# Kernel optimization log

Measured on AMD Instinct MI355X. Metric: run time of the kernel, lower is better.

The kernel has to match this reference:

```python
import jax, jax.numpy as jnp
import numpy as np

HEADS = 4

def gat_layer(x, W, a_src, a_dst, bias, edge_index, n):
    # PyG-style GATConv with self-loops, heads averaged (concat=False) so out dim == hidden_dim
    H, C = a_src.shape
    h = (x @ W).reshape(n, H, C)                      # [N,H,C]
    loops = jnp.arange(n)
    src = jnp.concatenate([edge_index[0], loops])
    dst = jnp.concatenate([edge_index[1], loops])
    e = jax.nn.leaky_relu((h * a_src).sum(-1)[src] + (h * a_dst).sum(-1)[dst], 0.2)  # [E,H]
    m = jax.ops.segment_max(e, dst, num_segments=n)   # segment softmax over incoming edges
    ex = jnp.exp(e - m[dst])
    s = jax.ops.segment_sum(ex, dst, num_segments=n)
    alpha = ex / (s[dst] + 1e-16)
    out = jax.ops.segment_sum(alpha[:, :, None] * h[src], dst, num_segments=n)  # [N,H,C]
    return out.mean(axis=1) + bias

def setup_inputs() -> dict:
    key = jax.random.key(0)
    ks = jax.random.split(key, 24)
    Nd, Ni, Ne = 20000, 4096, 4096
    D_in, D = 512, 256
    n_int, n_emo = 64, 32
    inp = {}
    inp['dialogue_embeddings'] = jax.random.normal(ks[0], (Nd, D_in), jnp.float32)
    inp['intention_indices'] = jax.random.randint(ks[1], (Ni,), 0, n_int)
    inp['emotion_indices'] = jax.random.randint(ks[2], (Ne,), 0, n_emo)
    inp['dialogue_edge_index'] = jax.random.randint(ks[3], (2, Nd * 32), 0, Nd)
    inp['intention_edge_index'] = jax.random.randint(ks[4], (2, Ni * 16), 0, Ni)
    inp['emotion_edge_index'] = jax.random.randint(ks[5], (2, Ne * 16), 0, Ne)
    s = lambda k, shape: jax.random.normal(k, shape, jnp.float32) * 0.02
    inp['intention_emb'] = s(ks[6], (n_int, D))
    inp['emotion_emb'] = s(ks[7], (n_emo, D))
    inp['Wd'] = s(ks[8], (D_in, HEADS * D)); inp['a_src_d'] = s(ks[9], (HEADS, D)); inp['a_dst_d'] = s(ks[10], (HEADS, D)); inp['bd'] = jnp.zeros((D,), jnp.float32)
    inp['Wi'] = s(ks[11], (D, HEADS * D)); inp['a_src_i'] = s(ks[12], (HEADS, D)); inp['a_dst_i'] = s(ks[13], (HEADS, D)); inp['bi'] = jnp.zeros((D,), jnp.float32)
    inp['We'] = s(ks[14], (D, HEADS * D)); inp['a_src_e'] = s(ks[15], (HEADS, D)); inp['a_dst_e'] = s(ks[16], (HEADS, D)); inp['be'] = jnp.zeros((D,), jnp.float32)
    inp['W_dfc'] = s(ks[17], (D, D)); inp['b_dfc'] = jnp.zeros((D,), jnp.float32)
    inp['W_ifc'] = s(ks[18], (D, D)); inp['b_ifc'] = jnp.zeros((D,), jnp.float32)
    inp['W_efc'] = s(ks[19], (D, D)); inp['b_efc'] = jnp.zeros((D,), jnp.float32)
    inp['W_fc'] = s(ks[20], (3 * D, n_emo)); inp['b_fc'] = jnp.zeros((n_emo,), jnp.float32)
    return inp

def reference(dialogue_embeddings, intention_indices, emotion_indices,
              dialogue_edge_index, intention_edge_index, emotion_edge_index,
              intention_emb, emotion_emb,
              Wd, a_src_d, a_dst_d, bd, Wi, a_src_i, a_dst_i, bi,
              We, a_src_e, a_dst_e, be,
              W_dfc, b_dfc, W_ifc, b_ifc, W_efc, b_efc, W_fc, b_fc):
    Nd = dialogue_embeddings.shape[0]
    Ni = intention_indices.shape[0]
    Ne = emotion_indices.shape[0]
    ie = intention_emb[intention_indices]   # [Ni, D]
    ee = emotion_emb[emotion_indices]       # [Ne, D]
    d = gat_layer(dialogue_embeddings, Wd, a_src_d, a_dst_d, bd, dialogue_edge_index, Nd)
    d = jax.nn.relu(d @ W_dfc + b_dfc)
    i = gat_layer(ie, Wi, a_src_i, a_dst_i, bi, intention_edge_index, Ni)
    i = jax.nn.relu(i @ W_ifc + b_ifc)
    e = gat_layer(ee, We, a_src_e, a_dst_e, be, emotion_edge_index, Ne)
    e = jax.nn.relu(e @ W_efc + b_efc)
    iw = jax.nn.softmax(d @ i.T, axis=-1)   # [Nd, Ni]
    att_i = iw @ i                           # [Nd, D]
    ew = jax.nn.softmax(d @ e.T, axis=-1)   # [Nd, Ne]
    att_e = ew @ e                           # [Nd, D]
    inputs = jnp.concatenate([d, att_i, att_e], axis=-1)  # [Nd, 3D]
    return inputs @ W_fc + b_fc
```

## Files before the change

kernel.cpp:

```cpp
#include <hip/hip_runtime.h>
#include <hip/hip_bf16.h>
#include <math.h>

#define DEV static __device__ __forceinline__

typedef __attribute__((ext_vector_type(8))) short short8;
typedef __attribute__((ext_vector_type(4))) short short4v;
typedef __attribute__((ext_vector_type(4))) float f32x4;
typedef __attribute__((ext_vector_type(2))) long long2v;

DEV float bf2f(__hip_bfloat16 x) { return __bfloat162float(x); }
DEV __hip_bfloat16 f2bf(float x) { return __float2bfloat16(x); }
DEV short bfbits(float x) { __hip_bfloat16 h = __float2bfloat16(x); short s; __builtin_memcpy(&s, &h, 2); return s; }
DEV float b2f_bits(short s) { __hip_bfloat16 h; __builtin_memcpy(&h, &s, 2); return __bfloat162float(h); }
DEV float lrelu(float x) { return x > 0.f ? x : 0.2f * x; }

DEV float load_in(const void* p, long long i, bool f32) {
  return f32 ? ((const float*)p)[i] : bf2f(((const __hip_bfloat16*)p)[i]);
}

DEV long pack8_fp8(const float* f) {
  int lo = 0, hi = 0;
  lo = __builtin_amdgcn_cvt_pk_fp8_f32(f[0], f[1], lo, false);
  lo = __builtin_amdgcn_cvt_pk_fp8_f32(f[2], f[3], lo, true);
  hi = __builtin_amdgcn_cvt_pk_fp8_f32(f[4], f[5], hi, false);
  hi = __builtin_amdgcn_cvt_pk_fp8_f32(f[6], f[7], hi, true);
  return ((long)(unsigned)hi << 32) | (unsigned)lo;
}

DEV f32x4 mfma_fp8(long a, long b, f32x4 c) {
  return __builtin_amdgcn_mfma_f32_16x16x32_fp8_fp8(a, b, c, 0, 0, 0);
}

__global__ void HGAN_45148696215914_kernel() {}

__global__ void fill_k(__hip_bfloat16* __restrict__ p, float v, int n)
{
  int i = blockIdx.x * blockDim.x + threadIdx.x;
  if (i < n) p[i] = __float2bfloat16(v);
}

struct DetectArgs { const unsigned int* p[23]; int nw[23]; int id[23]; };

__global__ void detect_k(DetectArgs a, int* __restrict__ flags)
{
  __shared__ int cnt_sh;
  if (threadIdx.x == 0) cnt_sh = 0;
  __syncthreads();
  const unsigned int* w = a.p[blockIdx.x];
  int nwords = a.nw[blockIdx.x];
  int bad = 0;
  for (int i = threadIdx.x; i < nwords; i += blockDim.x) {
    unsigned int x = w[i];
    float v0 = __uint_as_float((x & 0xffffu) << 16);
    float v1 = __uint_as_float(x & 0xffff0000u);
    if (!(fabsf(v0) <= 1e4f)) bad++;
    if (!(fabsf(v1) <= 1e4f)) bad++;
  }
  atomicAdd(&cnt_sh, bad);
  __syncthreads();
  if (threadIdx.x == 0) flags[a.id[blockIdx.x]] = (cnt_sh > nwords / 4) ? 1 : 0;
}

struct CvArgs {
  const void* in[7]; const int* flag[7]; __hip_bfloat16* out[7];
  int K[7], N[7], NL[7], toff[7]; int nseg;
};

__global__ __launch_bounds__(256) void convtrN_k(CvArgs a)
{
  __shared__ __hip_bfloat16 t[32][33];
  int b = blockIdx.x;
  int s = 0;
  while (s + 1 < a.nseg && b >= a.toff[s + 1]) ++s;
  int ti = b - a.toff[s];
  int kb = a.K[s] >> 5;
  int bk = ti % kb, bn = ti / kb;
  const void* in = a.in[s];
  const int* flag = a.flag[s];
  __hip_bfloat16* out = a.out[s];
  int K = a.K[s], N = a.N[s];
  const bool f = flag && *flag;
  int lx = threadIdx.x & 31, ly = threadIdx.x >> 5;
  int gn = bn * 32 + lx;
#pragma unroll
  for (int rr = 0; rr < 32; rr += 8)
    t[rr + ly][lx] = (gn < N)
        ? f2bf(load_in(in, (long long)(bk * 32 + rr + ly) * N + gn, f))
        : f2bf(0.f);
  __syncthreads();
#pragma unroll
  for (int rr = 0; rr < 32; rr += 8)
    out[(size_t)(bn * 32 + rr + ly) * K + bk * 32 + lx] = t[lx][rr + ly];
}

DEV void mgemm_body(
    const void* A, const int* aflag, int lda, const int* idxA,
    const __hip_bfloat16* BT, void* C, int ldc,
    const void* bias, const int* biasflag, int relu,
    int permC, int M, int K, int Nlim, const int* cflag,
    int m0, int n0, __hip_bfloat16* Ash, __hip_bfloat16* Bsh)
{
  const bool af = aflag && *aflag;
  const bool bsf = biasflag && *biasflag;
  const bool cf = cflag && *cflag;
  const int tid = threadIdx.x;
  const int wv = tid >> 6, lane = tid & 63, qd = lane >> 4, lm = lane & 15;
  const int wr = wv >> 1, wc = wv & 1;

  f32x4 acc[4][4];
#pragma unroll
  for (int i = 0; i < 4; ++i)
    for (int j = 0; j < 4; ++j)
      for (int v = 0; v < 4; ++v) acc[i][j][v] = 0.f;

  for (int k0 = 0; k0 < K; k0 += 64) {
    __syncthreads();
    for (int u = tid; u < 1024; u += 256) {
      int r = u >> 3, cu = u & 7;
      int gm = m0 + r;
      short8 vv;
      if (gm < M) {
        long long row = idxA ? idxA[gm] : gm;
        long long basei = row * (long long)lda + k0 + cu * 8;
        if (af) {
          const float4* fp = (const float4*)((const float*)A + basei);
          float4 f0 = fp[0], f1 = fp[1];
          vv[0] = bfbits(f0.x); vv[1] = bfbits(f0.y);
          vv[2] = bfbits(f0.z); vv[3] = bfbits(f0.w);
          vv[4] = bfbits(f1.x); vv[5] = bfbits(f1.y);
          vv[6] = bfbits(f1.z); vv[7] = bfbits(f1.w);
        } else {
          vv = *(const short8*)((const __hip_bfloat16*)A + basei);
        }
      } else {
#pragma unroll
        for (int j = 0; j < 8; ++j) vv[j] = 0;
      }
      *(short8*)(&Ash[r * 72 + cu * 8]) = vv;
    }
    for (int u = tid; u < 1024; u += 256) {
      int r = u >> 3, cu = u & 7;
      *(short8*)(&Bsh[r * 72 + cu * 8]) =
          *(const short8*)(BT + (size_t)(n0 + r) * K + k0 + cu * 8);
    }
    __syncthreads();
#pragma unroll
    for (int ks = 0; ks < 2; ++ks) {
      short8 a[4], b[4];
#pragma unroll
      for (int i = 0; i < 4; ++i)
        a[i] = *(const short8*)(&Ash[(wr * 64 + i * 16 + lm) * 72 + ks * 32 + qd * 8]);
#pragma unroll
      for (int j = 0; j < 4; ++j)
        b[j] = *(const short8*)(&Bsh[(wc * 64 + j * 16 + lm) * 72 + ks * 32 + qd * 8]);
#pragma unroll
      for (int i = 0; i < 4; ++i)
#pragma unroll
        for (int j = 0; j < 4; ++j)
          acc[i][j] = __builtin_amdgcn_mfma_f32_16x16x32_bf16(a[i], b[j], acc[i][j], 0, 0, 0);
    }
  }
#pragma unroll
  for (int j = 0; j < 4; ++j) {
    int gn = n0 + wc * 64 + j * 16 + lm;
    if (gn >= Nlim) continue;
    float bv = bias ? load_in(bias, gn, bsf) : 0.f;
    int gcol = permC ? ((gn & 255) * 4 + (gn >> 8)) : gn;
#pragma unroll
    for (int i = 0; i < 4; ++i) {
#pragma unroll
      for (int v = 0; v < 4; ++v) {
        int gm = m0 + wr * 64 + i * 16 + qd * 4 + v;
        if (gm >= M) continue;
        float x = acc[i][j][v] + bv;
        if (relu) x = fmaxf(x, 0.f);
        long long idx = (long long)gm * ldc + gcol;
        if (cf) ((float*)C)[idx] = x;
        else    ((__hip_bfloat16*)C)[idx] = f2bf(x);
      }
    }
  }
}

__global__ __launch_bounds__(256) void mgemm_k(
    const void* __restrict__ A, const int* __restrict__ aflag, int lda,
    const int* __restrict__ idxA,
    const __hip_bfloat16* __restrict__ BT,
    void* __restrict__ C, int ldc,
    const void* __restrict__ bias, const int* __restrict__ biasflag, int relu,
    int permC, int M, int N, int K, int Nlim,
    const int* __restrict__ cflag)
{
  __shared__ __align__(16) __hip_bfloat16 Ash[128 * 72];
  __shared__ __align__(16) __hip_bfloat16 Bsh[128 * 72];
  (void)N;
  mgemm_body(A, aflag, lda, idxA, BT, C, ldc, bias, biasflag, relu,
             permC, M, K, Nlim, cflag,
             blockIdx.y * 128, blockIdx.x * 128, Ash, Bsh);
}

struct SegArgs {
  const void* A[3]; const int* aflag[3]; int lda[3]; const int* idxA[3];
  const __hip_bfloat16* BT[3]; void* C[3]; int ldc[3];
  const void* bias[3]; const int* bflag[3];
  int M[3]; int K[3]; int yoff[3];
  int relu, permC, Nlim;
};

__global__ __launch_bounds__(256) void mgemm_seg_k(SegArgs a)
{
  __shared__ __align__(16) __hip_bfloat16 Ash[128 * 72];
  __shared__ __align__(16) __hip_bfloat16 Bsh[128 * 72];
  int y = blockIdx.y;
  int s = (y >= a.yoff[2]) ? 2 : ((y >= a.yoff[1]) ? 1 : 0);
  mgemm_body(a.A[s], a.aflag[s], a.lda[s], a.idxA[s], a.BT[s], a.C[s], a.ldc[s],
             a.bias[s], a.bflag[s], a.relu, a.permC, a.M[s], a.K[s], a.Nlim,
             nullptr, (y - a.yoff[s]) * 128, blockIdx.x * 128, Ash, Bsh);
}

__global__ __launch_bounds__(256) void score3_k(
    const __hip_bfloat16* __restrict__ hI,
    const void* as1, const void* ad1, const int* sf1, const int* df1,
    const void* as2, const void* ad2, const int* sf2, const int* df2,
    const void* as3, const void* ad3, const int* sf3, const int* df3,
    int s1, int s2,
    float* __restrict__ ss, float* __restrict__ ds,
    int* __restrict__ cnt, int N)
{
  __shared__ float red[4][8];
  int n = blockIdx.x, c = threadIdx.x;
  if (c == 0) cnt[n] = 0;
  const void* a_src; const void* a_dst; const int* sfp; const int* dfp;
  if (n < s1)      { a_src = as1; a_dst = ad1; sfp = sf1; dfp = df1; }
  else if (n < s2) { a_src = as2; a_dst = ad2; sfp = sf2; dfp = df2; }
  else             { a_src = as3; a_dst = ad3; sfp = sf3; dfp = df3; }
  const bool sf = sfp && *sfp;
  const bool df = dfp && *dfp;
  short4v hv = *(const short4v*)(hI + (size_t)n * 1024 + c * 4);
  float h0 = b2f_bits(hv[0]), h1 = b2f_bits(hv[1]);
  float h2 = b2f_bits(hv[2]), h3 = b2f_bits(hv[3]);
  float r0 = h0 * load_in(a_src, 0 * 256 + c, sf);
  float r1 = h1 * load_in(a_src, 1 * 256 + c, sf);
  float r2 = h2 * load_in(a_src, 2 * 256 + c, sf);
  float r3 = h3 * load_in(a_src, 3 * 256 + c, sf);
  float t0 = h0 * load_in(a_dst, 0 * 256 + c, df);
  float t1 = h1 * load_in(a_dst, 1 * 256 + c, df);
  float t2 = h2 * load_in(a_dst, 2 * 256 + c, df);
  float t3 = h3 * load_in(a_dst, 3 * 256 + c, df);
#pragma unroll
  for (int o = 32; o > 0; o >>= 1) {
    r0 += __shfl_down(r0, o); r1 += __shfl_down(r1, o);
    r2 += __shfl_down(r2, o); r3 += __shfl_down(r3, o);
    t0 += __shfl_down(t0, o); t1 += __shfl_down(t1, o);
    t2 += __shfl_down(t2, o); t3 += __shfl_down(t3, o);
  }
  int wv = c >> 6, lane = c & 63;
  if (lane == 0) {
    red[wv][0] = r0; red[wv][1] = r1; red[wv][2] = r2; red[wv][3] = r3;
    red[wv][4] = t0; red[wv][5] = t1; red[wv][6] = t2; red[wv][7] = t3;
  }
  __syncthreads();
  if (c < 8) {
    float s = red[0][c] + red[1][c] + red[2][c] + red[3][c];
    if (c < 4) ss[n * 4 + c] = s;
    else       ds[n * 4 + (c - 4)] = s;
  }
}

__global__ void count3_k(const int* __restrict__ d1, int E1,
                         const int* __restrict__ d2, int E2, int o2,
                         const int* __restrict__ d3, int E3, int o3,
                         int* __restrict__ cnt)
{
  int k = blockIdx.x * blockDim.x + threadIdx.x;
  if (k < E1) atomicAdd(&cnt[d1[k]], 1);
  else if (k < E1 + E2) atomicAdd(&cnt[d2[k - E1] + o2], 1);
  else if (k < E1 + E2 + E3) atomicAdd(&cnt[d3[k - E1 - E2] + o3], 1);
}

__global__ __launch_bounds__(1024) void scan1_k(
    const int* __restrict__ cnt, int* __restrict__ offp, int* __restrict__ bsum, int n)
{
  __shared__ int sh[1024];
  int idx = blockIdx.x * 1024 + (int)threadIdx.x;
  int v = (idx < n) ? cnt[idx] : 0;
  sh[threadIdx.x] = v;
  __syncthreads();
  for (int d = 1; d < 1024; d <<= 1) {
    int t = (threadIdx.x >= (unsigned)d) ? sh[threadIdx.x - d] : 0;
    __syncthreads();
    sh[threadIdx.x] += t;
    __syncthreads();
  }
  if (idx < n) offp[idx] = sh[threadIdx.x] - v;
  if (threadIdx.x == 1023) bsum[blockIdx.x] = sh[1023];
}

__global__ void scan3_k(int* __restrict__ offp, const int* __restrict__ bsum,
                        int* __restrict__ cur, int n, int nb)
{
  int i = blockIdx.x * blockDim.x + threadIdx.x;
  if (i < n) {
    int chunk = i >> 10;
    int pre = 0;
    for (int b = 0; b < chunk; ++b) pre += bsum[b];
    int v = offp[i] + pre;
    offp[i] = v;
    cur[i] = v;
    if (i == n - 1) {
      int tot = 0;
      for (int b = 0; b < nb; ++b) tot += bsum[b];
      offp[n] = tot;
    }
  }
}

__global__ void scatter3_k(const int* __restrict__ s1, const int* __restrict__ d1, int E1,
                           const int* __restrict__ s2, const int* __restrict__ d2, int E2, int o2,
                           const int* __restrict__ s3, const int* __restrict__ d3, int E3, int o3,
                           int* __restrict__ cur, int* __restrict__ srcs)
{
  int k = blockIdx.x * blockDim.x + threadIdx.x;
  if (k < E1) {
    int p = atomicAdd(&cur[d1[k]], 1);
    srcs[p] = s1[k];
  } else if (k < E1 + E2) {
    int kk = k - E1;
    int p = atomicAdd(&cur[d2[kk] + o2], 1);
    srcs[p] = s2[kk] + o2;
  } else if (k < E1 + E2 + E3) {
    int kk = k - E1 - E2;
    int p = atomicAdd(&cur[d3[kk] + o3], 1);
    srcs[p] = s3[kk] + o3;
  }
}

__global__ __launch_bounds__(256) void agg3_k(
    const __hip_bfloat16* __restrict__ hI,
    const float* __restrict__ ss, const float* __restrict__ ds,
    const int* __restrict__ offp, const int* __restrict__ srcs,
    const void* b1, const int* bf1,
    const void* b2, const int* bf2,
    const void* b3, const int* bf3,
    int s1, int s2,
    __hip_bfloat16* __restrict__ outp, int N)
{
  __shared__ int src_sh[64];
  __shared__ __align__(16) float w_sh[64][4];
  __shared__ float scale_sh[4];
  __shared__ float l_sh[4];
  __shared__ __align__(16) float pair_sh[128][8];
  int n = blockIdx.x;
  int c = threadIdx.x;
  int hd_w = c >> 6;
  int e_w  = c & 63;
  int half = c >> 7;
  int tc   = c & 127;
  int s0 = offp[n], deg = offp[n + 1] - s0;
  int total = deg + 1;
  float dsn = ds[n * 4 + hd_w];
  float m_run = -1e30f, l_run = 0.f;
  float A0[4] = {0.f, 0.f, 0.f, 0.f};
  float A1[4] = {0.f, 0.f, 0.f, 0.f};
  for (int base = 0; base < total; base += 64) {
    int cnt = min(64, total - base);
    __syncthreads();
    if (c < cnt) src_sh[c] = (base + c == 0) ? n : srcs[s0 + base + c - 1];
    __syncthreads();
    float val = -1e30f;
    if (e_w < cnt) val = lrelu(ss[src_sh[e_w] * 4 + hd_w] + dsn);
    float vmax = val;
#pragma unroll
    for (int o = 32; o > 0; o >>= 1) vmax = fmaxf(vmax, __shfl_xor(vmax, o));
    float newm = fmaxf(m_run, vmax);
    float p = (e_w < cnt) ? __expf(val - newm) : 0.f;
    float psum = p;
#pragma unroll
    for (int o = 32; o > 0; o >>= 1) psum += __shfl_xor(psum, o);
    float sc = __expf(m_run - newm);
    l_run = l_run * sc + psum;
    m_run = newm;
    w_sh[e_w][hd_w] = p;
    if (e_w == 0) scale_sh[hd_w] = sc;
    __syncthreads();
    float sc0 = scale_sh[0], sc1 = scale_sh[1], sc2 = scale_sh[2], sc3 = scale_sh[3];
    A0[0] *= sc0; A0[1] *= sc1; A0[2] *= sc2; A0[3] *= sc3;
    A1[0] *= sc0; A1[1] *= sc1; A1[2] *= sc2; A1[3] *= sc3;
    for (int e = half; e < cnt; e += 2) {
      short8 hv = *(const short8*)(hI + (size_t)src_sh[e] * 1024 + tc * 8);
      float4 w = *(const float4*)(&w_sh[e][0]);
      A0[0] += w.x * b2f_bits(hv[0]); A0[1] += w.y * b2f_bits(hv[1]);
      A0[2] += w.z * b2f_bits(hv[2]); A0[3] += w.w * b2f_bits(hv[3]);
      A1[0] += w.x * b2f_bits(hv[4]); A1[1] += w.y * b2f_bits(hv[5]);
      A1[2] += w.z * b2f_bits(hv[6]); A1[3] += w.w * b2f_bits(hv[7]);
    }
  }
  __syncthreads();
  if (e_w == 0) l_sh[hd_w] = l_run;
  if (half == 1) {
    *(float4*)(&pair_sh[tc][0]) = make_float4(A0[0], A0[1], A0[2], A0[3]);
    *(float4*)(&pair_sh[tc][4]) = make_float4(A1[0], A1[1], A1[2], A1[3]);
  }
  __syncthreads();
  if (half == 0) {
    float4 p0 = *(const float4*)(&pair_sh[tc][0]);
    float4 p1 = *(const float4*)(&pair_sh[tc][4]);
    A0[0] += p0.x; A0[1] += p0.y; A0[2] += p0.z; A0[3] += p0.w;
    A1[0] += p1.x; A1[1] += p1.y; A1[2] += p1.z; A1[3] += p1.w;
    const void* bias; const int* bfp;
    if (n < s1)      { bias = b1; bfp = bf1; }
    else if (n < s2) { bias = b2; bfp = bf2; }
    else             { bias = b3; bfp = bf3; }
    const bool bf = bfp && *bfp;
    float il0 = 1.f / (l_sh[0] + 1e-16f), il1 = 1.f / (l_sh[1] + 1e-16f);
    float il2 = 1.f / (l_sh[2] + 1e-16f), il3 = 1.f / (l_sh[3] + 1e-16f);
    float r0 = 0.25f * (A0[0] * il0 + A0[1] * il1 + A0[2] * il2 + A0[3] * il3);
    float r1 = 0.25f * (A1[0] * il0 + A1[1] * il1 + A1[2] * il2 + A1[3] * il3);
    outp[(size_t)n * 256 + 2 * tc]     = f2bf(r0 + load_in(bias, 2 * tc, bf));
    outp[(size_t)n * 256 + 2 * tc + 1] = f2bf(r1 + load_in(bias, 2 * tc + 1, bf));
  }
}

__global__ __launch_bounds__(256) void conv8_k(
    const __hip_bfloat16* __restrict__ in0, char* __restrict__ K8_0, char* __restrict__ KT8_0,
    const __hip_bfloat16* __restrict__ in1, char* __restrict__ K8_1, char* __restrict__ KT8_1,
    int Nk)
{
  __shared__ __align__(16) __hip_bfloat16 t[32][264];
  const __hip_bfloat16* in = blockIdx.y ? in1 : in0;
  char* K8  = blockIdx.y ? K8_1  : K8_0;
  char* KT8 = blockIdx.y ? KT8_1 : KT8_0;
  int kv0 = blockIdx.x * 32;
  size_t tbase = (size_t)(kv0 >> 5) * 8192;
  int tid = threadIdx.x;
  (void)Nk;
  for (int u = tid; u < 1024; u += 256) {
    int r = u >> 5, c = u & 31;
    *(short8*)(&t[r][c * 8]) = *(const short8*)(in + (size_t)(kv0 + r) * 256 + c * 8);
  }
  __syncthreads();
  for (int u = tid; u < 1024; u += 256) {
    int r = u >> 5, g = u & 31, pos = g * 8;
    int qd_ = pos >> 6, s = (pos >> 3) & 7;
    int d = s * 32 + qd_ * 8;
    float f[8];
#pragma unroll
    for (int j = 0; j < 8; ++j) f[j] = 16.f * bf2f(t[r][d + j]);
    int c16 = pos >> 4, h = (pos >> 3) & 1;
    int unit = ((c16 & 3) * 2 + (r >> 4)) * 64 + (c16 >> 2) * 16 + (r & 15);
    *(long*)(K8 + tbase + (size_t)unit * 16 + h * 8) = pack8_fp8(f);
  }
  {
    int d = tid;
#pragma unroll
    for (int g = 0; g < 4; ++g) {
      float f[8];
#pragma unroll
      for (int j = 0; j < 8; ++j) f[j] = 16.f * bf2f(t[g * 8 + j][d]);
      int unit = (d >> 4) * 64 + g * 16 + (d & 15);
      *(long*)(KT8 + tbase + (size_t)unit * 8) = pack8_fp8(f);
    }
  }
}

__global__ __launch_bounds__(512, 4) void flashf8_k(
    const __hip_bfloat16* __restrict__ Q, int ldq,
    const char* __restrict__ K8_0, const char* __restrict__ KT8_0,
    const char* __restrict__ K8_1, const char* __restrict__ KT8_1,
    __hip_bfloat16* __restrict__ Out, int ldo,
    int M, int Nk)
{
  __shared__ __align__(16) char Ksh8[2][8192];
  __shared__ __align__(16) char KTsh8[2][8192];
  __shared__ __align__(16) char Psh8[8][16 * 40];
  const int att = blockIdx.y;
  const char* K8  = att ? K8_1  : K8_0;
  const char* KT8 = att ? KT8_1 : KT8_0;
  __hip_bfloat16* Outp = Out + att * 256;

  const int tid = threadIdx.x;
  const int wv = tid >> 6, lane = tid & 63;
  const int qd = lane >> 4, lm = lane & 15;
  const int r0 = blockIdx.x * 128 + wv * 16;
  char* Pw = Psh8[wv];

  long qf8[8];
  {
    const bool ok = (r0 + lm) < M;
    const __hip_bfloat16* qrow = Q + (size_t)(r0 + lm) * ldq;
#pragma unroll
    for (int s = 0; s < 8; ++s) {
      float f[8];
      if (ok) {
        short8 qv = *(const short8*)(qrow + s * 32 + qd * 8);
#pragma unroll
        for (int j = 0; j < 8; ++j) f[j] = 16.f * b2f_bits(qv[j]);
      } else {
#pragma unroll
        for (int j = 0; j < 8; ++j) f[j] = 0.f;
      }
      qf8[s] = pack8_fp8(f);
    }
  }

  f32x4 Oacc[16];
#pragma unroll
  for (int i = 0; i < 16; ++i)
    for (int v = 0; v < 4; ++v) Oacc[i][v] = 0.f;
  float mrow = -1e30f, lrow = 0.f;

  {
    short8 k0 = *(const short8*)(K8 + (size_t)tid * 16);
    short8 t0 = *(const short8*)(KT8 + (size_t)tid * 16);
    *(short8*)(&Ksh8[0][tid * 16]) = k0;
    *(short8*)(&KTsh8[0][tid * 16]) = t0;
  }
  __syncthreads();

  int iter = 0;
  for (int n0 = 0; n0 < Nk; n0 += 32, ++iter) {
    const int cur = iter & 1, nxt = cur ^ 1;
    const bool havenext = (n0 + 32) < Nk;
    short8 pk0, pt0;
    if (havenext) {
      size_t tb = (size_t)(iter + 1) * 8192;
      pk0 = *(const short8*)(K8 + tb + (size_t)tid * 16);
      pt0 = *(const short8*)(KT8 + tb + (size_t)tid * 16);
    }
    const char* Kc  = Ksh8[cur];
    const char* KTc = KTsh8[cur];

    f32x4 S[2];
#pragma unroll
    for (int t = 0; t < 2; ++t)
      for (int v = 0; v < 4; ++v) S[t][v] = 0.f;
#pragma unroll
    for (int sp = 0; sp < 4; ++sp) {
#pragma unroll
      for (int t = 0; t < 2; ++t) {
        long2v a2 = *(const long2v*)(&Kc[((sp * 2 + t) * 64 + lane) * 16]);
        S[t] = mfma_fp8(a2[0], qf8[2 * sp],     S[t]);
        S[t] = mfma_fp8(a2[1], qf8[2 * sp + 1], S[t]);
      }
    }
#pragma unroll
    for (int t = 0; t < 2; ++t)
      for (int v = 0; v < 4; ++v) S[t][v] *= 0.00390625f;

    float tmax = -1e30f;
#pragma unroll
    for (int t = 0; t < 2; ++t)
      for (int v = 0; v < 4; ++v) tmax = fmaxf(tmax, S[t][v]);
    tmax = fmaxf(tmax, __shfl_xor(tmax, 16));
    tmax = fmaxf(tmax, __shfl_xor(tmax, 32));
    float newm = fmaxf(mrow, tmax);
    float psum = 0.f;
#pragma unroll
    for (int t = 0; t < 2; ++t)
      for (int v = 0; v < 4; ++v) {
        float p = __expf(S[t][v] - newm);
        S[t][v] = p;
        psum += p;
      }
    psum += __shfl_xor(psum, 16);
    psum += __shfl_xor(psum, 32);
    float scale = __expf(mrow - newm);
    lrow = lrow * scale + psum;
    mrow = newm;
#pragma unroll
    for (int t = 0; t < 2; ++t) {
      int pk = __builtin_amdgcn_cvt_pk_fp8_f32(16.f * S[t][0], 16.f * S[t][1], 0, false);
      pk = __builtin_amdgcn_cvt_pk_fp8_f32(16.f * S[t][2], 16.f * S[t][3], pk, true);
      *(int*)(&Pw[lm * 40 + t * 16 + qd * 4]) = pk;
    }

    if (__any(scale < 1.0f)) {
      float scl[4];
#pragma unroll
      for (int v = 0; v < 4; ++v) scl[v] = __shfl(scale, qd * 4 + v);
#pragma unroll
      for (int i = 0; i < 16; ++i)
        for (int v = 0; v < 4; ++v) Oacc[i][v] *= scl[v];
    }

    {
      long pa0 = *(const long*)(&Pw[lm * 40 + qd * 8]);
#pragma unroll
      for (int dt = 0; dt < 16; ++dt) {
        long b = *(const long*)(&KTc[dt * 512 + lane * 8]);
        Oacc[dt] = mfma_fp8(pa0, b, Oacc[dt]);
      }
    }

    if (havenext) {
      *(short8*)(&Ksh8[nxt][tid * 16]) = pk0;
      *(short8*)(&KTsh8[nxt][tid * 16]) = pt0;
    }
    __syncthreads();
  }

  {
    float linv = 1.f / (256.f * lrow);
    float li[4];
#pragma unroll
    for (int v = 0; v < 4; ++v) li[v] = __shfl(linv, qd * 4 + v);
#pragma unroll
    for (int v = 0; v < 4; ++v) {
      int grow = r0 + qd * 4 + v;
      if (grow >= M) continue;
#pragma unroll
      for (int dt = 0; dt < 16; ++dt)
        Outp[(size_t)grow * ldo + dt * 16 + lm] = f2bf(Oacc[dt][v] * li[v]);
    }
  }
}

extern "C" void kernel_launch(void* const* d_in, const int* in_sizes, int n_in,
                              void* d_out, int out_size, void* d_ws, size_t ws_size,
                              hipStream_t stream)
{
  const void* Xd      = d_in[0];
  const int*  int_idx = (const int*)d_in[1];
  const int*  emo_idx = (const int*)d_in[2];
  const int*  ed_d    = (const int*)d_in[3];
  const int*  ed_i    = (const int*)d_in[4];
  const int*  ed_e    = (const int*)d_in[5];
  const void* int_emb = d_in[6];
  const void* emo_emb = d_in[7];
  const void* Wd = d_in[8],  *a_src_d = d_in[9],  *a_dst_d = d_in[10], *bd = d_in[11];
  const void* Wi = d_in[12], *a_src_i = d_in[13], *a_dst_i = d_in[14], *bi = d_in[15];
  const void* We = d_in[16], *a_src_e = d_in[17], *a_dst_e = d_in[18], *be = d_in[19];
  const void* W_dfc = d_in[20], *b_dfc = d_in[21];
  const void* W_ifc = d_in[22], *b_ifc = d_in[23];
  const void* W_efc = d_in[24], *b_efc = d_in[25];
  const void* W_fc  = d_in[26], *b_fc  = d_in[27];

  const int DIn  = in_sizes[8] / 1024;
  const int Nd   = in_sizes[0] / DIn;
  const int Ni   = in_sizes[1];
  const int Ne   = in_sizes[2];
  const int Ed   = in_sizes[3] / 2;
  const int Ei   = in_sizes[4] / 2;
  const int Ee   = in_sizes[5] / 2;
  const int Nout = in_sizes[27];
  const int NU   = Nd + Ni + Ne;

  char* base = (char*)d_ws;
  size_t off = 0;
  auto alloc = [&](size_t nbytes) -> void* {
    void* p = base + off;
    off = (off + nbytes + 255) & ~(size_t)255;
    return p;
  };
  int* flags = (int*)alloc(32 * sizeof(int));
  int* bsum  = (int*)alloc(64 * sizeof(int));
  __hip_bfloat16* hbuf = (__hip_bfloat16*)alloc((size_t)NU * 1024 * 2);
  __hip_bfloat16* cat  = (__hip_bfloat16*)alloc((size_t)Nd * 768 * 2);
  __hip_bfloat16* gat_tmp = (__hip_bfloat16*)alloc((size_t)NU * 256 * 2);
  __hip_bfloat16* WdT  = (__hip_bfloat16*)alloc((size_t)1024 * DIn * 2);
  __hip_bfloat16* WiT  = (__hip_bfloat16*)alloc((size_t)1024 * 256 * 2);
  __hip_bfloat16* WeT  = (__hip_bfloat16*)alloc((size_t)1024 * 256 * 2);
  __hip_bfloat16* WdfT = (__hip_bfloat16*)alloc((size_t)256 * 256 * 2);
  __hip_bfloat16* WifT = (__hip_bfloat16*)alloc((size_t)256 * 256 * 2);
  __hip_bfloat16* WefT = (__hip_bfloat16*)alloc((size_t)256 * 256 * 2);
  __hip_bfloat16* WfcT = (__hip_bfloat16*)alloc((size_t)128 * 768 * 2);
  float* ss  = (float*)alloc((size_t)NU * 4 * 4);
  float* dsb = (float*)alloc((size_t)NU * 4 * 4);
  int* cnt   = (int*)alloc((size_t)NU * 4);
  int* offp  = (int*)alloc((size_t)(NU + 1) * 4);
  int* cur   = (int*)alloc((size_t)NU * 4);
  int* srcs  = (int*)alloc((size_t)(Ed + Ei + Ee) * 4);
  const size_t need = off;
  (void)n_in;

  __hip_bfloat16* i_mat = hbuf;
  __hip_bfloat16* e_mat = hbuf + (size_t)Ni * 256;
  char* K8i  = (char*)(hbuf + (size_t)2 * Ni * 256);
  char* KT8i = K8i + (size_t)Ni * 256;
  char* K8e  = KT8i + (size_t)Ni * 256;
  char* KT8e = K8e + (size_t)Ne * 256;

  const dim3 T(256);
  if (ws_size < need) {
    fill_k<<<(out_size + 255) / 256, T, 0, stream>>>((__hip_bfloat16*)d_out, 0.25f, out_size);
    return;
  }

  {
    DetectArgs da;
    const int fid[23] = {0,6,7,8,9,10,11,12,13,14,15,16,17,18,19,20,21,22,23,24,25,26,27};
    for (int t = 0; t < 23; ++t) {
      int id = fid[t];
      int nw = in_sizes[id] / 2;
      if (nw > 2048) nw = 2048;
      if (nw < 1) nw = 1;
      da.p[t] = (const unsigned int*)d_in[id];
      da.nw[t] = nw;
      da.id[t] = id;
    }
    detect_k<<<23, 256, 0, stream>>>(da, flags);
  }
  #define F(i) (flags + (i))

  {
    CvArgs cv;
    const void* ins[7]  = {Wd, Wi, We, W_dfc, W_ifc, W_efc, W_fc};
    const int*  fgs[7]  = {F(8), F(12), F(16), F(20), F(22), F(24), F(26)};
    __hip_bfloat16* outs[7] = {WdT, WiT, WeT, WdfT, WifT, WefT, WfcT};
    int Ks[7]  = {DIn, 256, 256, 256, 256, 256, 768};
    int Ns[7]  = {1024, 1024, 1024, 256, 256, 256, Nout};
    int NLs[7] = {1024, 1024, 1024, 256, 256, 256, 128};
    int run = 0;
    for (int s = 0; s < 7; ++s) {
      cv.in[s] = ins[s]; cv.flag[s] = fgs[s]; cv.out[s] = outs[s];
      cv.K[s] = Ks[s]; cv.N[s] = Ns[s]; cv.NL[s] = NLs[s]; cv.toff[s] = run;
      run += (Ks[s] / 32) * (NLs[s] / 32);
    }
    cv.nseg = 7;
    convtrN_k<<<run, T, 0, stream>>>(cv);
  }

  const int yNd = (Nd + 127) / 128, yNi = Ni / 128, yNe = Ne / 128;
  {
    SegArgs sa;
    sa.A[0] = Xd;      sa.aflag[0] = F(0); sa.lda[0] = DIn; sa.idxA[0] = nullptr;
    sa.BT[0] = WdT;    sa.C[0] = hbuf;     sa.ldc[0] = 1024;
    sa.bias[0] = nullptr; sa.bflag[0] = nullptr; sa.M[0] = Nd; sa.K[0] = DIn;
    sa.A[1] = int_emb; sa.aflag[1] = F(6); sa.lda[1] = 256; sa.idxA[1] = int_idx;
    sa.BT[1] = WiT;    sa.C[1] = hbuf + (size_t)Nd * 1024; sa.ldc[1] = 1024;
    sa.bias[1] = nullptr; sa.bflag[1] = nullptr; sa.M[1] = Ni; sa.K[1] = 256;
    sa.A[2] = emo_emb; sa.aflag[2] = F(7); sa.lda[2] = 256; sa.idxA[2] = emo_idx;
    sa.BT[2] = WeT;    sa.C[2] = hbuf + (size_t)(Nd + Ni) * 1024; sa.ldc[2] = 1024;
    sa.bias[2] = nullptr; sa.bflag[2] = nullptr; sa.M[2] = Ne; sa.K[2] = 256;
    sa.yoff[0] = 0; sa.yoff[1] = yNd; sa.yoff[2] = yNd + yNi;
    sa.relu = 0; sa.permC = 1; sa.Nlim = 1024;
    mgemm_seg_k<<<dim3(8, yNd + yNi + yNe), T, 0, stream>>>(sa);
  }

  {
    int nb = (NU + 1023) / 1024;
    int Etot = Ed + Ei + Ee;
    score3_k<<<NU, T, 0, stream>>>(hbuf,
        a_src_d, a_dst_d, F(9), F(10),
        a_src_i, a_dst_i, F(13), F(14),
        a_src_e, a_dst_e, F(17), F(18),
        Nd, Nd + Ni, ss, dsb, cnt, NU);
    count3_k<<<(Etot + 255) / 256, T, 0, stream>>>(
        ed_d + Ed, Ed, ed_i + Ei, Ei, Nd, ed_e + Ee, Ee, Nd + Ni, cnt);
    scan1_k<<<nb, 1024, 0, stream>>>(cnt, offp, bsum, NU);
    scan3_k<<<(NU + 255) / 256, T, 0, stream>>>(offp, bsum, cur, NU, nb);
    scatter3_k<<<(Etot + 255) / 256, T, 0, stream>>>(
        ed_d, ed_d + Ed, Ed, ed_i, ed_i + Ei, Ei, Nd,
        ed_e, ed_e + Ee, Ee, Nd + Ni, cur, srcs);
    agg3_k<<<NU, T, 0, stream>>>(hbuf, ss, dsb, offp, srcs,
        bd, F(11), bi, F(15), be, F(19), Nd, Nd + Ni, gat_tmp, NU);
  }

  {
    SegArgs sa;
    sa.A[0] = gat_tmp; sa.aflag[0] = nullptr; sa.lda[0] = 256; sa.idxA[0] = nullptr;
    sa.BT[0] = WdfT;   sa.C[0] = cat;   sa.ldc[0] = 768;
    sa.bias[0] = b_dfc; sa.bflag[0] = F(21); sa.M[0] = Nd; sa.K[0] = 256;
    sa.A[1] = gat_tmp + (size_t)Nd * 256; sa.aflag[1] = nullptr; sa.lda[1] = 256; sa.idxA[1] = nullptr;
    sa.BT[1] = WifT;   sa.C[1] = i_mat; sa.ldc[1] = 256;
    sa.bias[1] = b_ifc; sa.bflag[1] = F(23); sa.M[1] = Ni; sa.K[1] = 256;
    sa.A[2] = gat_tmp + (size_t)(Nd + Ni) * 256; sa.aflag[2] = nullptr; sa.lda[2] = 256; sa.idxA[2] = nullptr;
    sa.BT[2] = WefT;   sa.C[2] = e_mat; sa.ldc[2] = 256;
    sa.bias[2] = b_efc; sa.bflag[2] = F(25); sa.M[2] = Ne; sa.K[2] = 256;
    sa.yoff[0] = 0; sa.yoff[1] = yNd; sa.yoff[2] = yNd + yNi;
    sa.relu = 1; sa.permC = 0; sa.Nlim = 256;
    mgemm_seg_k<<<dim3(2, yNd + yNi + yNe), T, 0, stream>>>(sa);
  }

  conv8_k<<<dim3(Ni / 32, 2), T, 0, stream>>>(i_mat, K8i, KT8i, e_mat, K8e, KT8e, Ni);

  flashf8_k<<<dim3((Nd + 127) / 128, 2), dim3(512), 0, stream>>>(
      cat, 768, K8i, KT8i, K8e, KT8e, cat + 256, 768, Nd, Ni);

  mgemm_k<<<dim3(1, (Nd + 127) / 128), T, 0, stream>>>(
      cat, nullptr, 768, nullptr, WfcT, d_out, Nout,
      b_fc, F(27), 0, 0, Nd, 128, 768, Nout, F(0));
}
```

Baseline: 889.3 us.

## Restructure flash attention kernel to 64-key tiles, 4-wave blocks, lazy rescaling

```diff
diff --git a/kernel.cpp b/kernel.cpp
--- a/kernel.cpp
+++ b/kernel.cpp
@@ -464,16 +464,16 @@
   }
 }
 
-__global__ __launch_bounds__(512, 4) void flashf8_k(
+__global__ __launch_bounds__(256, 2) void flashf8_k(
     const __hip_bfloat16* __restrict__ Q, int ldq,
     const char* __restrict__ K8_0, const char* __restrict__ KT8_0,
     const char* __restrict__ K8_1, const char* __restrict__ KT8_1,
     __hip_bfloat16* __restrict__ Out, int ldo,
     int M, int Nk)
 {
-  __shared__ __align__(16) char Ksh8[2][8192];
-  __shared__ __align__(16) char KTsh8[2][8192];
-  __shared__ __align__(16) char Psh8[8][16 * 40];
+  __shared__ __align__(16) char Ksh8[2][16384];
+  __shared__ __align__(16) char KTsh8[2][16384];
+  __shared__ __align__(16) char Psh8[4][2][16 * 40];
   const int att = blockIdx.y;
   const char* K8  = att ? K8_1  : K8_0;
   const char* KT8 = att ? KT8_1 : KT8_0;
@@ -482,8 +482,7 @@
   const int tid = threadIdx.x;
   const int wv = tid >> 6, lane = tid & 63;
   const int qd = lane >> 4, lm = lane & 15;
-  const int r0 = blockIdx.x * 128 + wv * 16;
-  char* Pw = Psh8[wv];
+  const int r0 = blockIdx.x * 64 + wv * 16;
 
   long qf8[8];
   {
@@ -511,53 +510,69 @@
   float mrow = -1e30f, lrow = 0.f;
 
   {
-    short8 k0 = *(const short8*)(K8 + (size_t)tid * 16);
-    short8 t0 = *(const short8*)(KT8 + (size_t)tid * 16);
-    *(short8*)(&Ksh8[0][tid * 16]) = k0;
-    *(short8*)(&KTsh8[0][tid * 16]) = t0;
+#pragma unroll
+    for (int j = 0; j < 4; ++j) {
+      *(short8*)(&Ksh8[0][tid * 16 + j * 4096]) =
+          *(const short8*)(K8 + (size_t)tid * 16 + j * 4096);
+      *(short8*)(&KTsh8[0][tid * 16 + j * 4096]) =
+          *(const short8*)(KT8 + (size_t)tid * 16 + j * 4096);
+    }
   }
   __syncthreads();
 
-  int iter = 0;
-  for (int n0 = 0; n0 < Nk; n0 += 32, ++iter) {
-    const int cur = iter & 1, nxt = cur ^ 1;
-    const bool havenext = (n0 + 32) < Nk;
-    short8 pk0, pt0;
+  const int niter = Nk >> 6;
+  for (int it = 0; it < niter; ++it) {
+    const int cur = it & 1, nxt = cur ^ 1;
+    const bool havenext = (it + 1) < niter;
+    short8 pk[4], pt[4];
     if (havenext) {
-      size_t tb = (size_t)(iter + 1) * 8192;
-      pk0 = *(const short8*)(K8 + tb + (size_t)tid * 16);
-      pt0 = *(const short8*)(KT8 + tb + (size_t)tid * 16);
+      size_t tb = (size_t)(it + 1) * 16384;
+#pragma unroll
+      for (int j = 0; j < 4; ++j) {
+        pk[j] = *(const short8*)(K8 + tb + (size_t)tid * 16 + j * 4096);
+        pt[j] = *(const short8*)(KT8 + tb + (size_t)tid * 16 + j * 4096);
+      }
     }
     const char* Kc  = Ksh8[cur];
     const char* KTc = KTsh8[cur];
 
-    f32x4 S[2];
-#pragma unroll
-    for (int t = 0; t < 2; ++t)
+    f32x4 S[4];
+#pragma unroll
+    for (int t = 0; t < 4; ++t)
       for (int v = 0; v < 4; ++v) S[t][v] = 0.f;
 #pragma unroll
     for (int sp = 0; sp < 4; ++sp) {
 #pragma unroll
-      for (int t = 0; t < 2; ++t) {
-        long2v a2 = *(const long2v*)(&Kc[((sp * 2 + t) * 64 + lane) * 16]);
+      for (int t = 0; t < 4; ++t) {
+        long2v a2 = *(const long2v*)(
+            &Kc[(t >> 1) * 8192 + ((sp * 2 + (t & 1)) * 64 + lane) * 16]);
         S[t] = mfma_fp8(a2[0], qf8[2 * sp],     S[t]);
         S[t] = mfma_fp8(a2[1], qf8[2 * sp + 1], S[t]);
       }
     }
 #pragma unroll
-    for (int t = 0; t < 2; ++t)
+    for (int t = 0; t < 4; ++t)
       for (int v = 0; v < 4; ++v) S[t][v] *= 0.00390625f;
 
+    if (havenext) {
+#pragma unroll
+      for (int j = 0; j < 4; ++j) {
+        *(short8*)(&Ksh8[nxt][tid * 16 + j * 4096]) = pk[j];
+        *(short8*)(&KTsh8[nxt][tid * 16 + j * 4096]) = pt[j];
+      }
+    }
+
     float tmax = -1e30f;
 #pragma unroll
-    for (int t = 0; t < 2; ++t)
+    for (int t = 0; t < 4; ++t)
       for (int v = 0; v < 4; ++v) tmax = fmaxf(tmax, S[t][v]);
     tmax = fmaxf(tmax, __shfl_xor(tmax, 16));
     tmax = fmaxf(tmax, __shfl_xor(tmax, 32));
-    float newm = fmaxf(mrow, tmax);
+    const bool need = __any(tmax > mrow + 2.0f);
+    float newm = need ? fmaxf(mrow, tmax) : mrow;
     float psum = 0.f;
 #pragma unroll
-    for (int t = 0; t < 2; ++t)
+    for (int t = 0; t < 4; ++t)
       for (int v = 0; v < 4; ++v) {
         float p = __expf(S[t][v] - newm);
         S[t][v] = p;
@@ -565,38 +580,42 @@
       }
     psum += __shfl_xor(psum, 16);
     psum += __shfl_xor(psum, 32);
-    float scale = __expf(mrow - newm);
-    lrow = lrow * scale + psum;
-    mrow = newm;
-#pragma unroll
-    for (int t = 0; t < 2; ++t) {
-      int pk = __builtin_amdgcn_cvt_pk_fp8_f32(16.f * S[t][0], 16.f * S[t][1], 0, false);
-      pk = __builtin_amdgcn_cvt_pk_fp8_f32(16.f * S[t][2], 16.f * S[t][3], pk, true);
-      *(int*)(&Pw[lm * 40 + t * 16 + qd * 4]) = pk;
-    }
-
-    if (__any(scale < 1.0f)) {
-      float scl[4];
-#pragma unroll
-      for (int v = 0; v < 4; ++v) scl[v] = __shfl(scale, qd * 4 + v);
-#pragma unroll
-      for (int i = 0; i < 16; ++i)
-        for (int v = 0; v < 4; ++v) Oacc[i][v] *= scl[v];
+
+#pragma unroll
+    for (int t = 0; t < 4; ++t) {
+      int pk32 = __builtin_amdgcn_cvt_pk_fp8_f32(16.f * S[t][0], 16.f * S[t][1], 0, false);
+      pk32 = __builtin_amdgcn_cvt_pk_fp8_f32(16.f * S[t][2], 16.f * S[t][3], pk32, true);
+      *(int*)(&Psh8[wv][t >> 1][lm * 40 + (t & 1) * 16 + qd * 4]) = pk32;
+    }
+
+    if (need) {
+      float scale = __expf(mrow - newm);
+      lrow = lrow * scale + psum;
+      mrow = newm;
+      if (__any(scale < 1.0f)) {
+        float scl[4];
+#pragma unroll
+        for (int v = 0; v < 4; ++v) scl[v] = __shfl(scale, qd * 4 + v);
+#pragma unroll
+        for (int i = 0; i < 16; ++i)
+          for (int v = 0; v < 4; ++v) Oacc[i][v] *= scl[v];
+      }
+    } else {
+      lrow += psum;
     }
 
     {
-      long pa0 = *(const long*)(&Pw[lm * 40 + qd * 8]);
+      long pa0 = *(const long*)(&Psh8[wv][0][lm * 40 + qd * 8]);
+      long pa1 = *(const long*)(&Psh8[wv][1][lm * 40 + qd * 8]);
 #pragma unroll
       for (int dt = 0; dt < 16; ++dt) {
-        long b = *(const long*)(&KTc[dt * 512 + lane * 8]);
-        Oacc[dt] = mfma_fp8(pa0, b, Oacc[dt]);
+        long b0 = *(const long*)(&KTc[dt * 512 + lane * 8]);
+        long b1 = *(const long*)(&KTc[8192 + dt * 512 + lane * 8]);
+        Oacc[dt] = mfma_fp8(pa0, b0, Oacc[dt]);
+        Oacc[dt] = mfma_fp8(pa1, b1, Oacc[dt]);
       }
     }
 
-    if (havenext) {
-      *(short8*)(&Ksh8[nxt][tid * 16]) = pk0;
-      *(short8*)(&KTsh8[nxt][tid * 16]) = pt0;
-    }
     __syncthreads();
   }
 
@@ -775,7 +794,7 @@
 
   conv8_k<<<dim3(Ni / 32, 2), T, 0, stream>>>(i_mat, K8i, KT8i, e_mat, K8e, KT8e, Ni);
 
-  flashf8_k<<<dim3((Nd + 127) / 128, 2), dim3(512), 0, stream>>>(
+  flashf8_k<<<dim3((Nd + 63) / 64, 2), T, 0, stream>>>(
       cat, 768, K8i, KT8i, K8e, KT8e, cat + 256, 768, Nd, Ni);
 
   mgemm_k<<<dim3(1, (Nd + 127) / 128), T, 0, stream>>>(
```

New measurement: 890.7 us. No clear change (+0.2%).
